# Kernel tuning notes

Hardware: AMD Instinct MI355X
Metric: run time of the kernel (lower is better)

Reference implementation:

```python
import jax, jax.numpy as jnp
import numpy as np

N_AGT, N_CTX, E, D, NC = 100000, 10000, 1000000, 128, 2


def _gn(x, w, b, eps=1e-5):
    # GroupNorm(num_groups=1) on (N, C): normalize over channels, affine.
    m = jnp.mean(x, axis=-1, keepdims=True)
    v = jnp.mean((x - m) ** 2, axis=-1, keepdims=True)
    return (x - m) * jax.lax.rsqrt(v + eps) * w + b


def setup_inputs() -> dict:
    key = jax.random.key(0)
    ks = jax.random.split(key, 16)
    s = 0.05  # weight scale
    return {
        "agts": jax.random.normal(ks[0], (N_AGT, D), jnp.float32),
        "ctx": jax.random.normal(ks[1], (N_CTX, D), jnp.float32),
        "agt_ctrs": jax.random.normal(ks[2], (N_AGT, NC), jnp.float32),
        "ctx_ctrs": jax.random.normal(ks[3], (N_CTX, NC), jnp.float32),
        "hi": jax.random.randint(ks[4], (E,), 0, N_AGT, jnp.int32),
        "wi": jax.random.randint(ks[5], (E,), 0, N_CTX, jnp.int32),
        "dist_w1": jax.random.normal(ks[6], (D, NC), jnp.float32) * s,
        "dist_b1": jnp.zeros((D,), jnp.float32),
        "dist_w2": jax.random.normal(ks[7], (D, D), jnp.float32) * s,
        "dist_gw": jnp.ones((D,), jnp.float32),
        "dist_gb": jnp.zeros((D,), jnp.float32),
        "q_w": jax.random.normal(ks[8], (D, D), jnp.float32) * s,
        "q_gw": jnp.ones((D,), jnp.float32),
        "q_gb": jnp.zeros((D,), jnp.float32),
        "ctx_w1": jax.random.normal(ks[9], (D, 3 * D), jnp.float32) * s,
        "ctx_gw": jnp.ones((D,), jnp.float32),
        "ctx_gb": jnp.zeros((D,), jnp.float32),
        "ctx_w2": jax.random.normal(ks[10], (D, D), jnp.float32) * s,
        "agt_w": jax.random.normal(ks[11], (D, D), jnp.float32) * s,
        "norm_gw": jnp.ones((D,), jnp.float32),
        "norm_gb": jnp.zeros((D,), jnp.float32),
        "lin_w": jax.random.normal(ks[12], (D, D), jnp.float32) * s,
        "lin_gw": jnp.ones((D,), jnp.float32),
        "lin_gb": jnp.zeros((D,), jnp.float32),
    }


def reference(agts, ctx, agt_ctrs, ctx_ctrs, hi, wi,
              dist_w1, dist_b1, dist_w2, dist_gw, dist_gb,
              q_w, q_gw, q_gb,
              ctx_w1, ctx_gw, ctx_gb, ctx_w2,
              agt_w, norm_gw, norm_gb,
              lin_w, lin_gw, lin_gb):
    res = agts
    # per-edge relative displacement: [E, 2]
    d = agt_ctrs[hi] - ctx_ctrs[wi]
    # dist MLP: Linear(2,128)+ReLU, Linear(128,128,nobias)+GN+ReLU
    d = jax.nn.relu(d @ dist_w1.T + dist_b1)
    d = jax.nn.relu(_gn(d @ dist_w2.T, dist_gw, dist_gb))
    # query: Linear(128,128,nobias)+GN+ReLU on gathered agents
    q = jax.nn.relu(_gn(agts[hi] @ q_w.T, q_gw, q_gb))
    # concat-MLP over edges: [E, 384] -> [E, 128]
    c = jnp.concatenate([d, q, ctx[wi]], axis=1)
    c = jax.nn.relu(_gn(c @ ctx_w1.T, ctx_gw, ctx_gb))
    c = c @ ctx_w2.T
    # agent transform + index_add scatter of edge messages
    a = agts @ agt_w.T
    a = a.at[hi].add(c)
    a = jax.nn.relu(_gn(a, norm_gw, norm_gb))
    a = _gn(a @ lin_w.T, lin_gw, lin_gb)  # Linear block with act=False
    a = jax.nn.relu(a + res)
    return a
```

## Files before the change

kernel.cpp:

```cpp
#include <hip/hip_runtime.h>
#include <stdint.h>


#define N_AGT 100000
#define N_CTX 10000
#define NE    1000000
#define D     128

typedef __attribute__((ext_vector_type(8))) __bf16 bf16x8;
typedef __attribute__((ext_vector_type(4))) float f32x4;
typedef __attribute__((ext_vector_type(4))) unsigned int uint32x4;
typedef __attribute__((ext_vector_type(8))) unsigned short ushort8;

__device__ __forceinline__ float bf_lo(uint32_t u){ return __uint_as_float(u << 16); }
__device__ __forceinline__ float bf_hi(uint32_t u){ return __uint_as_float(u & 0xFFFF0000u); }
__device__ __forceinline__ uint16_t f2bf(float f){
  uint32_t u = __float_as_uint(f);
  u += 0x7FFFu + ((u >> 16) & 1u);
  return (uint16_t)(u >> 16);
}
__device__ __forceinline__ uint16_t f2bf_fast(float f){
  const __bf16 b = (__bf16)f;
  return __builtin_bit_cast(uint16_t, b);
}
__device__ __forceinline__ float bf2f(uint16_t v){ return __uint_as_float(((uint32_t)v) << 16); }

__device__ __forceinline__ f32x4 mfma16(bf16x8 a, bf16x8 b, f32x4 c){
  return __builtin_amdgcn_mfma_f32_16x16x32_bf16(a, b, c, 0, 0, 0);
}

__device__ __forceinline__ void wave_lgkm0(){
  asm volatile("s_waitcnt lgkmcnt(0)" ::: "memory");
  __builtin_amdgcn_sched_barrier(0);
}


__device__ __forceinline__ void stage_wsz(char* dst, const float* __restrict__ W,
                                          int rs, int co, int tid, int nthr){
  for (int idx = tid; idx < 128*16; idx += nthr){
    const int row = idx >> 4, ch = idx & 15;
    const float4 f0 = *(const float4*)(W + (size_t)row*rs + co + ch*8);
    const float4 f1 = *(const float4*)(W + (size_t)row*rs + co + ch*8 + 4);
    ushort8 u;
    u[0]=f2bf(f0.x); u[1]=f2bf(f0.y); u[2]=f2bf(f0.z); u[3]=f2bf(f0.w);
    u[4]=f2bf(f1.x); u[5]=f2bf(f1.y); u[6]=f2bf(f1.z); u[7]=f2bf(f1.w);
    *(uint32x4*)(dst + row*256 + ((ch*16) ^ ((row&7)<<4))) = __builtin_bit_cast(uint32x4, u);
  }
}

__device__ __forceinline__ bf16x8 ldfrag(const char* base, int row, int cb){
  return __builtin_bit_cast(bf16x8,
      *(const uint32x4*)(base + row*256 + (cb ^ ((row&7)<<4))));
}

#define SCAN_B  256
#define SCAN_CH ((N_AGT + SCAN_B - 1) / SCAN_B)

__global__ __launch_bounds__(256) void k_hist(const int* __restrict__ hi,
                                              int* __restrict__ cnt){
  for (int i = blockIdx.x*256 + threadIdx.x; i < NE; i += gridDim.x*256)
    atomicAdd(&cnt[hi[i]], 1);
}

__global__ __launch_bounds__(256) void k_scan1(const int* __restrict__ cnt,
                                               int* __restrict__ bsum){
  __shared__ int red[4];
  const int b = blockIdx.x, t = threadIdx.x;
  const int lo = b*SCAN_CH, hiX = min(lo + SCAN_CH, N_AGT);
  int s = 0;
  for (int i = lo + t; i < hiX; i += 256) s += cnt[i];
  #pragma unroll
  for (int m = 1; m < 64; m <<= 1) s += __shfl_xor(s, m);
  if ((t & 63) == 0) red[t >> 6] = s;
  __syncthreads();
  if (t == 0) bsum[b] = red[0] + red[1] + red[2] + red[3];
}

__global__ __launch_bounds__(SCAN_B) void k_scan2(int* __restrict__ bsum){
  __shared__ int part[SCAN_B];
  const int t = threadIdx.x;
  const int v = bsum[t];
  part[t] = v;
  __syncthreads();
  for (int ofs = 1; ofs < SCAN_B; ofs <<= 1){
    const int add = (t >= ofs) ? part[t - ofs] : 0;
    __syncthreads();
    part[t] += add;
    __syncthreads();
  }
  bsum[t] = part[t] - v;
}

__global__ __launch_bounds__(256) void k_scan3(int* __restrict__ cnt,
                                               const int* __restrict__ bsum){
  __shared__ int tpart[256];
  const int b = blockIdx.x, t = threadIdx.x;
  const int lo = b*SCAN_CH, hiX = min(lo + SCAN_CH, N_AGT);
  const int per = (SCAN_CH + 255) / 256;
  const int s0 = lo + t*per, s1 = min(s0 + per, hiX);
  int s = 0;
  for (int i = s0; i < s1; i++) s += cnt[i];
  tpart[t] = s;
  __syncthreads();
  for (int ofs = 1; ofs < 256; ofs <<= 1){
    const int add = (t >= ofs) ? tpart[t - ofs] : 0;
    __syncthreads();
    tpart[t] += add;
    __syncthreads();
  }
  int run = bsum[b] + tpart[t] - s;
  for (int i = s0; i < s1; i++){
    const int c = cnt[i];
    cnt[i] = run;
    run += c;
  }
}

__global__ __launch_bounds__(256) void k_scatter(const int* __restrict__ hi,
                                                 const int* __restrict__ wi,
                                                 int* __restrict__ cur,
                                                 uint64_t* __restrict__ hw){
  for (int i = blockIdx.x*256 + threadIdx.x; i < NE; i += gridDim.x*256){
    const int h = hi[i];
    const int pos = atomicAdd(&cur[h], 1);
    hw[pos] = ((uint64_t)(uint32_t)wi[i] << 32) | (uint32_t)h;
  }
}

#define NWIT (NE/16)

__device__ __forceinline__ void mm16(const char* T, const char* W,
                                     int llo, int lhi, f32x4 acc[8]){
  bf16x8 a[4];
  #pragma unroll
  for (int kt = 0; kt < 4; kt++) a[kt] = ldfrag(T, llo, kt*64 + lhi*16);
  #pragma unroll
  for (int nt = 0; nt < 8; nt++){
    acc[nt] = (f32x4)0.f;
    #pragma unroll
    for (int kt = 0; kt < 4; kt++){
      const bf16x8 b = ldfrag(W, nt*16 + llo, kt*64 + lhi*16);
      acc[nt] = mfma16(a[kt], b, acc[nt]);
    }
  }
}

__device__ __forceinline__ void gn_reg(f32x4 acc[8], const float gw[8],
                                       const float gb[8]){
  float s[4] = {0,0,0,0}, ss[4] = {0,0,0,0};
  #pragma unroll
  for (int nt = 0; nt < 8; nt++)
    #pragma unroll
    for (int r = 0; r < 4; r++){
      const float v = acc[nt][r];
      s[r] += v; ss[r] += v*v;
    }
  #pragma unroll
  for (int m = 1; m < 16; m <<= 1)
    #pragma unroll
    for (int r = 0; r < 4; r++){
      s[r] += __shfl_xor(s[r], m);
      ss[r] += __shfl_xor(ss[r], m);
    }
  float mean[4], rstd[4];
  #pragma unroll
  for (int r = 0; r < 4; r++){
    mean[r] = s[r]*(1.f/128.f);
    const float var = ss[r]*(1.f/128.f) - mean[r]*mean[r];
    rstd[r] = rsqrtf(var + 1e-5f);
  }
  #pragma unroll
  for (int nt = 0; nt < 8; nt++)
    #pragma unroll
    for (int r = 0; r < 4; r++)
      acc[nt][r] = fmaxf((acc[nt][r]-mean[r])*rstd[r]*gw[nt] + gb[nt], 0.f);
}

__device__ __forceinline__ void scat16(char* T, const f32x4 acc[8],
                                       int llo, int lhi){
  #pragma unroll
  for (int nt = 0; nt < 8; nt++)
    #pragma unroll
    for (int r = 0; r < 4; r++){
      const int row = lhi*4 + r;
      *(uint16_t*)(T + row*256 + ((2*(nt*16 + llo)) ^ ((row&7)<<4))) =
          f2bf_fast(acc[nt][r]);
    }
}

__global__ __launch_bounds__(512, 2) void k_edge_mfma(
    const float* __restrict__ agt_ctrs, const float* __restrict__ ctx_ctrs,
    const uint32_t* __restrict__ hw32,
    const float* __restrict__ dist_w1, const float* __restrict__ dist_b1,
    const float* __restrict__ dist_gw, const float* __restrict__ dist_gb,
    const float* __restrict__ ctx_gw, const float* __restrict__ ctx_gb,
    const float* __restrict__ dist_w2, const float* __restrict__ ctx_w1,
    const float* __restrict__ ctx_w2,
    const uint16_t* __restrict__ QW, const uint16_t* __restrict__ CtxP,
    float* __restrict__ A0){
  extern __shared__ __align__(16) char smem[];
  const int tid  = threadIdx.x;
  const int wave = tid >> 6, lane = tid & 63;
  const int lhi  = lane >> 4, llo = lane & 15;

  stage_wsz(smem,         dist_w2, 128, 0, tid, 512);
  stage_wsz(smem + 32768, ctx_w1,  384, 0, tid, 512);
  stage_wsz(smem + 65536, ctx_w2,  128, 0, tid, 512);

  char* T = smem + 98304 + wave*4096;

  const int c0 = llo*8;
  float w1x[8], w1y[8], b1v[8];
  #pragma unroll
  for (int j = 0; j < 8; j++){
    w1x[j] = dist_w1[(c0+j)*2 + 0];
    w1y[j] = dist_w1[(c0+j)*2 + 1];
    b1v[j] = dist_b1[c0+j];
  }
  float dgwr[8], dgbr[8], cgwr[8], cgbr[8];
  #pragma unroll
  for (int nt = 0; nt < 8; nt++){
    dgwr[nt] = dist_gw[nt*16 + llo]; dgbr[nt] = dist_gb[nt*16 + llo];
    cgwr[nt] = ctx_gw[nt*16 + llo];  cgbr[nt] = ctx_gb[nt*16 + llo];
  }
  __syncthreads();

  const int wid = blockIdx.x*8 + wave;
  const int nw  = gridDim.x*8;

  for (int i = wid; i < NWIT; i += nw){
    const int base = i*16;
    const uint32x4 q0 = *(const uint32x4*)&hw32[2*(base + lhi*4)];
    const uint32x4 q1 = *(const uint32x4*)&hw32[2*(base + lhi*4) + 4];
    const int hh[4] = {(int)q0[0], (int)q0[2], (int)q1[0], (int)q1[2]};
    const int ww[4] = {(int)q0[1], (int)q0[3], (int)q1[1], (int)q1[3]};
    const uint2 p2 = *(const uint2*)&hw32[2*(base + llo)];
    const int h2 = (int)p2.x, w2 = (int)p2.y;
    uint32x4 qql[4], qcl[4];
    #pragma unroll
    for (int k = 0; k < 4; k++){
      qql[k] = *(const uint32x4*)&QW  [(size_t)h2*D + lhi*32 + k*8];
      qcl[k] = *(const uint32x4*)&CtxP[(size_t)w2*D + lhi*32 + k*8];
    }
    #pragma unroll
    for (int j = 0; j < 4; j++){
      const float2 ac = *(const float2*)&agt_ctrs[(size_t)hh[j]*2];
      const float2 cc = *(const float2*)&ctx_ctrs[(size_t)ww[j]*2];
      const float dx = ac.x - cc.x, dy = ac.y - cc.y;
      ushort8 u;
      #pragma unroll
      for (int c = 0; c < 8; c++)
        u[c] = f2bf_fast(fmaxf(fmaf(dx, w1x[c], fmaf(dy, w1y[c], b1v[c])), 0.f));
      const int row = lhi*4 + j;
      *(uint32x4*)(T + row*256 + ((llo*16) ^ ((row&7)<<4))) =
          __builtin_bit_cast(uint32x4, u);
    }
    wave_lgkm0();
    f32x4 acc[8];
    mm16(T, smem, llo, lhi, acc);
    gn_reg(acc, dgwr, dgbr);
    wave_lgkm0();
    scat16(T, acc, llo, lhi);
    wave_lgkm0();
    mm16(T, smem + 32768, llo, lhi, acc);
    ushort8 qs[4];
    #pragma unroll
    for (int k = 0; k < 4; k++){
      const ushort8 a = __builtin_bit_cast(ushort8, qql[k]);
      const ushort8 b = __builtin_bit_cast(ushort8, qcl[k]);
      ushort8 v;
      #pragma unroll
      for (int j = 0; j < 8; j++) v[j] = f2bf_fast(bf2f(a[j]) + bf2f(b[j]));
      qs[k] = v;
    }
    wave_lgkm0();
    #pragma unroll
    for (int k = 0; k < 4; k++)
      *(uint32x4*)(T + llo*256 + (((lhi*64) + k*16) ^ ((llo&7)<<4))) =
          __builtin_bit_cast(uint32x4, qs[k]);
    wave_lgkm0();
    #pragma unroll
    for (int nt = 0; nt < 8; nt++)
      #pragma unroll
      for (int r = 0; r < 4; r++){
        const int row = lhi*4 + r;
        const uint16_t q = *(const uint16_t*)(T + row*256 +
            ((2*(nt*16 + llo)) ^ ((row&7)<<4)));
        acc[nt][r] += bf2f(q);
      }
    gn_reg(acc, cgwr, cgbr);
    wave_lgkm0();
    scat16(T, acc, llo, lhi);
    wave_lgkm0();
    mm16(T, smem + 65536, llo, lhi, acc);
    wave_lgkm0();
    scat16(T, acc, llo, lhi);
    wave_lgkm0();
    {
      const int cA = lane, cB = lane + 64;
      float runA = 0.f, runB = 0.f;
      int hprev = __shfl(h2, 0);
      #pragma unroll
      for (int k = 0; k < 16; k++){
        const int hk = __shfl(h2, k);
        if (hk != hprev){
          atomicAdd(&A0[(size_t)hprev*D + cA], runA);
          atomicAdd(&A0[(size_t)hprev*D + cB], runB);
          runA = 0.f; runB = 0.f; hprev = hk;
        }
        runA += bf2f(*(const uint16_t*)(T + k*256 + ((2*cA) ^ ((k&7)<<4))));
        runB += bf2f(*(const uint16_t*)(T + k*256 + ((2*cB) ^ ((k&7)<<4))));
      }
      atomicAdd(&A0[(size_t)hprev*D + cA], runA);
      atomicAdd(&A0[(size_t)hprev*D + cB], runB);
    }
  }
}

__device__ __forceinline__ void mm_stage(const char* xb, const char* wm, int wv,
                                         int llo, int lhi, f32x4 acc[3][2]){
  #pragma unroll
  for (int kt = 0; kt < 4; kt++){
    const int cb = kt*64 + lhi*16;
    const bf16x8 b0 = ldfrag(wm, wv*32 + llo,      cb);
    const bf16x8 b1 = ldfrag(wm, wv*32 + 16 + llo, cb);
    #pragma unroll
    for (int mt = 0; mt < 3; mt++){
      const bf16x8 a = ldfrag(xb, mt*16 + llo, cb);
      acc[mt][0] = mfma16(a, b0, acc[mt][0]);
      acc[mt][1] = mfma16(a, b1, acc[mt][1]);
    }
  }
}

__device__ __forceinline__ void scat_acc(char* xb, const f32x4 acc[3][2],
                                         int wv, int llo, int lhi){
  #pragma unroll
  for (int mt = 0; mt < 3; mt++)
    #pragma unroll
    for (int ntl = 0; ntl < 2; ntl++)
      #pragma unroll
      for (int r = 0; r < 4; r++){
        const int m = mt*16 + lhi*4 + r;
        const int n = wv*32 + ntl*16 + llo;
        *(uint16_t*)(xb + m*256 + ((n*2) ^ ((m&7)<<4))) = f2bf(acc[mt][ntl][r]);
      }
}

__device__ __forceinline__ void gn_rowpass(char* xb, const int rr[3], int llo,
                                           const float gw[8], const float gb[8]){
  #pragma unroll
  for (int i = 0; i < 3; i++){
    const int row = rr[i];
    char* p = xb + row*256 + ((llo*16) ^ ((row&7)<<4));
    ushort8 u = __builtin_bit_cast(ushort8, *(const uint32x4*)p);
    float f[8]; float s = 0.f, ss = 0.f;
    #pragma unroll
    for (int j = 0; j < 8; j++){ f[j] = bf2f(u[j]); s += f[j]; ss += f[j]*f[j]; }
    #pragma unroll
    for (int m = 1; m < 16; m <<= 1){ s += __shfl_xor(s, m); ss += __shfl_xor(ss, m); }
    const float mean = s*(1.f/128.f);
    const float var  = ss*(1.f/128.f) - mean*mean;
    const float rstd = rsqrtf(var + 1e-5f);
    #pragma unroll
    for (int j = 0; j < 8; j++){
      const float g = fmaxf((f[j]-mean)*rstd*gw[j] + gb[j], 0.f);
      u[j] = f2bf(g);
    }
    *(uint32x4*)p = __builtin_bit_cast(uint32x4, u);
  }
}

#define NITER_A ((N_AGT + 95) / 96)

__global__ __launch_bounds__(512, 2) void k_agent_pre_mfma(
    const float* __restrict__ agts, const float* __restrict__ q_w,
    const float* __restrict__ ctx_w1, const float* __restrict__ agt_w,
    const float* __restrict__ q_gw, const float* __restrict__ q_gb,
    uint16_t* __restrict__ QW, float* __restrict__ A0){
  extern __shared__ __align__(16) char smem[];
  const int tid  = threadIdx.x;
  const int wave = tid >> 6, lane = tid & 63;
  const int grp  = wave >> 2, wv = wave & 3;
  const int lhi  = lane >> 4, llo = lane & 15;

  stage_wsz(smem,         q_w,    128, 0,   tid, 512);
  stage_wsz(smem + 32768, agt_w,  128, 0,   tid, 512);
  stage_wsz(smem + 65536, ctx_w1, 384, 128, tid, 512);

  char* xb = smem + 98304 + grp*12288;
  const int c0 = llo*8;
  float qgw[8], qgb[8];
  #pragma unroll
  for (int j = 0; j < 8; j++){ qgw[j] = q_gw[c0+j]; qgb[j] = q_gb[c0+j]; }
  __syncthreads();

  const int tg = tid & 255;
  int rr[3];
  #pragma unroll
  for (int i = 0; i < 3; i++) rr[i] = wv*12 + i*4 + lhi;

  for (int it = blockIdx.x; it < NITER_A; it += gridDim.x){
    const int rbase = it*96 + grp*48;
    for (int idx = tg; idx < 48*32; idx += 256){
      const int row = idx >> 5, c4 = idx & 31;
      int gr = rbase + row; if (gr >= N_AGT) gr = N_AGT - 1;
      const float4 f = *(const float4*)(agts + (size_t)gr*D + c4*4);
      const uint32_t lo = ((uint32_t)f2bf(f.y) << 16) | (uint32_t)f2bf(f.x);
      const uint32_t hi2 = ((uint32_t)f2bf(f.w) << 16) | (uint32_t)f2bf(f.z);
      *(uint2*)(xb + row*256 + ((c4*8) ^ ((row&7)<<4))) = make_uint2(lo, hi2);
    }
    __syncthreads();
    f32x4 acc[3][2];
    #pragma unroll
    for (int mt = 0; mt < 3; mt++){ acc[mt][0] = (f32x4)0.f; acc[mt][1] = (f32x4)0.f; }
    mm_stage(xb, smem + 32768, wv, llo, lhi, acc);
    #pragma unroll
    for (int mt = 0; mt < 3; mt++)
      #pragma unroll
      for (int ntl = 0; ntl < 2; ntl++)
        #pragma unroll
        for (int r = 0; r < 4; r++){
          const int m = mt*16 + lhi*4 + r;
          if (rbase + m < N_AGT){
            const int n = wv*32 + ntl*16 + llo;
            A0[(size_t)(rbase + m)*D + n] = acc[mt][ntl][r];
          }
        }
    #pragma unroll
    for (int mt = 0; mt < 3; mt++){ acc[mt][0] = (f32x4)0.f; acc[mt][1] = (f32x4)0.f; }
    mm_stage(xb, smem, wv, llo, lhi, acc);
    __syncthreads();
    scat_acc(xb, acc, wv, llo, lhi);
    __syncthreads();
    gn_rowpass(xb, rr, llo, qgw, qgb);
    __syncthreads();
    #pragma unroll
    for (int mt = 0; mt < 3; mt++){ acc[mt][0] = (f32x4)0.f; acc[mt][1] = (f32x4)0.f; }
    mm_stage(xb, smem + 65536, wv, llo, lhi, acc);
    __syncthreads();
    scat_acc(xb, acc, wv, llo, lhi);
    __syncthreads();
    #pragma unroll
    for (int i = 0; i < 3; i++){
      const int row = rr[i], gr = rbase + row;
      if (gr < N_AGT){
        const uint32x4 u = *(const uint32x4*)(xb + row*256 + ((llo*16) ^ ((row&7)<<4)));
        *(uint32x4*)(QW + (size_t)gr*D + c0) = u;
      }
    }
    __syncthreads();
  }
}

__global__ __launch_bounds__(512, 4) void k_post_mfma(
    float* __restrict__ A0, const float* __restrict__ agts,
    const float* __restrict__ lin_w,
    const float* __restrict__ norm_gw, const float* __restrict__ norm_gb,
    const float* __restrict__ lin_gw, const float* __restrict__ lin_gb){
  extern __shared__ __align__(16) char smem[];
  const int tid  = threadIdx.x;
  const int wave = tid >> 6, lane = tid & 63;
  const int grp  = wave >> 2, wv = wave & 3;
  const int lhi  = lane >> 4, llo = lane & 15;

  stage_wsz(smem, lin_w, 128, 0, tid, 512);
  char* xb = smem + 32768 + grp*12288;
  const int c0 = llo*8;
  float ngw[8], ngb[8], lgw[8], lgb[8];
  #pragma unroll
  for (int j = 0; j < 8; j++){
    ngw[j] = norm_gw[c0+j]; ngb[j] = norm_gb[c0+j];
    lgw[j] = lin_gw[c0+j];  lgb[j] = lin_gb[c0+j];
  }
  __syncthreads();

  int rr[3];
  #pragma unroll
  for (int i = 0; i < 3; i++) rr[i] = wv*12 + i*4 + lhi;

  for (int it = blockIdx.x; it < NITER_A; it += gridDim.x){
    const int rbase = it*96 + grp*48;
    #pragma unroll
    for (int i = 0; i < 3; i++){
      const int row = rr[i];
      int gr = rbase + row; if (gr >= N_AGT) gr = N_AGT - 1;
      const float4 a0 = *(const float4*)(A0 + (size_t)gr*D + c0);
      const float4 a1 = *(const float4*)(A0 + (size_t)gr*D + c0 + 4);
      float f[8] = {a0.x,a0.y,a0.z,a0.w,a1.x,a1.y,a1.z,a1.w};
      float s = 0.f, ss = 0.f;
      #pragma unroll
      for (int j = 0; j < 8; j++){ s += f[j]; ss += f[j]*f[j]; }
      #pragma unroll
      for (int m = 1; m < 16; m <<= 1){ s += __shfl_xor(s, m); ss += __shfl_xor(ss, m); }
      const float mean = s*(1.f/128.f);
      const float var  = ss*(1.f/128.f) - mean*mean;
      const float rstd = rsqrtf(var + 1e-5f);
      ushort8 u;
      #pragma unroll
      for (int j = 0; j < 8; j++)
        u[j] = f2bf(fmaxf((f[j]-mean)*rstd*ngw[j] + ngb[j], 0.f));
      *(uint32x4*)(xb + row*256 + ((llo*16) ^ ((row&7)<<4))) =
          __builtin_bit_cast(uint32x4, u);
    }
    __syncthreads();
    f32x4 acc[3][2];
    #pragma unroll
    for (int mt = 0; mt < 3; mt++){ acc[mt][0] = (f32x4)0.f; acc[mt][1] = (f32x4)0.f; }
    mm_stage(xb, smem, wv, llo, lhi, acc);
    __syncthreads();
    scat_acc(xb, acc, wv, llo, lhi);
    __syncthreads();
    #pragma unroll
    for (int i = 0; i < 3; i++){
      const int row = rr[i];
      const char* p = xb + row*256 + ((llo*16) ^ ((row&7)<<4));
      const ushort8 u = __builtin_bit_cast(ushort8, *(const uint32x4*)p);
      float f[8]; float s = 0.f, ss = 0.f;
      #pragma unroll
      for (int j = 0; j < 8; j++){ f[j] = bf2f(u[j]); s += f[j]; ss += f[j]*f[j]; }
      #pragma unroll
      for (int m = 1; m < 16; m <<= 1){ s += __shfl_xor(s, m); ss += __shfl_xor(ss, m); }
      const float mean = s*(1.f/128.f);
      const float var  = ss*(1.f/128.f) - mean*mean;
      const float rstd = rsqrtf(var + 1e-5f);
      const int gr = rbase + row;
      if (gr < N_AGT){
        const float4 r0 = *(const float4*)(agts + (size_t)gr*D + c0);
        const float4 r1 = *(const float4*)(agts + (size_t)gr*D + c0 + 4);
        const float res[8] = {r0.x,r0.y,r0.z,r0.w,r1.x,r1.y,r1.z,r1.w};
        float o[8];
        float4 o0, o1;
        #pragma unroll
        for (int j = 0; j < 8; j++)
          o[j] = fmaxf((f[j]-mean)*rstd*lgw[j] + lgb[j] + res[j], 0.f);
        o0.x=o[0]; o0.y=o[1]; o0.z=o[2]; o0.w=o[3];
        o1.x=o[4]; o1.y=o[5]; o1.z=o[6]; o1.w=o[7];
        *(float4*)(A0 + (size_t)gr*D + c0)     = o0;
        *(float4*)(A0 + (size_t)gr*D + c0 + 4) = o1;
      }
    }
    __syncthreads();
  }
}

__device__ __forceinline__ void stage_w4(uint32_t* wp, const float* __restrict__ W,
                                         int rs, int co, int tid, int nthr){
  for (int idx = tid; idx < 32*128; idx += nthr){
    int p2 = idx & 31, o = idx >> 5;
    const float4 f = *(const float4*)(W + (size_t)o*rs + co + p2*4);
    uint32_t lo = ((uint32_t)f2bf(f.y) << 16) | (uint32_t)f2bf(f.x);
    uint32_t hi = ((uint32_t)f2bf(f.w) << 16) | (uint32_t)f2bf(f.z);
    *(uint2*)&wp[(p2*128 + o)*2] = make_uint2(lo, hi);
  }
}

__device__ __forceinline__ float dot128(const uint32_t* wp, const float* xb, int o){
  float acc = 0.f;
  #pragma unroll 8
  for (int p2 = 0; p2 < 32; p2++){
    const uint2 w = *(const uint2*)&wp[(p2*128 + o)*2];
    const float4 x = *(const float4*)&xb[p2*4];
    acc += x.x*bf_lo(w.x) + x.y*bf_hi(w.x) + x.z*bf_lo(w.y) + x.w*bf_hi(w.y);
  }
  return acc;
}

__global__ __launch_bounds__(128) void k_ctx(const float* __restrict__ ctx,
                                             const float* __restrict__ ctx_w1,
                                             uint16_t* __restrict__ CtxP){
  __shared__ __align__(16) uint32_t wc[32*128*2];
  __shared__ __align__(16) float xbuf[128];
  const int tid = threadIdx.x;
  stage_w4(wc, ctx_w1, 384, 256, tid, 128);
  __syncthreads();
  for (int row = blockIdx.x; row < N_CTX; row += gridDim.x){
    __syncthreads();
    xbuf[tid] = ctx[(size_t)row*D + tid];
    __syncthreads();
    const float acc = dot128(wc, xbuf, tid);
    CtxP[(size_t)row*D + tid] = f2bf(acc);
  }
}

extern "C" void kernel_launch(void* const* d_in, const int* in_sizes, int n_in,
                              void* d_out, int out_size, void* d_ws, size_t ws_size,
                              hipStream_t stream){
  const float* agts     = (const float*)d_in[0];
  const float* ctx      = (const float*)d_in[1];
  const float* agt_ctrs = (const float*)d_in[2];
  const float* ctx_ctrs = (const float*)d_in[3];
  const int*   hi       = (const int*)d_in[4];
  const int*   wi       = (const int*)d_in[5];
  const float* dist_w1  = (const float*)d_in[6];
  const float* dist_b1  = (const float*)d_in[7];
  const float* dist_w2  = (const float*)d_in[8];
  const float* dist_gw  = (const float*)d_in[9];
  const float* dist_gb  = (const float*)d_in[10];
  const float* q_w      = (const float*)d_in[11];
  const float* q_gw     = (const float*)d_in[12];
  const float* q_gb     = (const float*)d_in[13];
  const float* ctx_w1   = (const float*)d_in[14];
  const float* ctx_gw   = (const float*)d_in[15];
  const float* ctx_gb   = (const float*)d_in[16];
  const float* ctx_w2   = (const float*)d_in[17];
  const float* agt_w    = (const float*)d_in[18];
  const float* norm_gw  = (const float*)d_in[19];
  const float* norm_gb  = (const float*)d_in[20];
  const float* lin_w    = (const float*)d_in[21];
  const float* lin_gw   = (const float*)d_in[22];
  const float* lin_gb   = (const float*)d_in[23];

  uint16_t* QW   = (uint16_t*)d_ws;
  uint16_t* CtxP = QW + (size_t)N_AGT * D;
  int*      cnt  = (int*)((char*)d_ws + 28160000);
  int*      bsum = (int*)((char*)d_ws + 28560000);
  uint64_t* hw   = (uint64_t*)((char*)d_ws + 28561024);
  float*    A0   = (float*)d_out;

  const int EDGE_LDS = 131072;
  const int APRE_LDS = 122880;
  const int POST_LDS = 57344;
  hipFuncSetAttribute((const void*)k_edge_mfma,
                      hipFuncAttributeMaxDynamicSharedMemorySize, EDGE_LDS);
  hipFuncSetAttribute((const void*)k_agent_pre_mfma,
                      hipFuncAttributeMaxDynamicSharedMemorySize, APRE_LDS);
  hipFuncSetAttribute((const void*)k_post_mfma,
                      hipFuncAttributeMaxDynamicSharedMemorySize, POST_LDS);

  hipMemsetAsync(cnt, 0, (size_t)N_AGT*4, stream);
  k_hist<<<2048, 256, 0, stream>>>(hi, cnt);
  k_scan1<<<SCAN_B, 256, 0, stream>>>(cnt, bsum);
  k_scan2<<<1, SCAN_B, 0, stream>>>(bsum);
  k_scan3<<<SCAN_B, 256, 0, stream>>>(cnt, bsum);
  k_scatter<<<2048, 256, 0, stream>>>(hi, wi, cnt, hw);

  k_ctx<<<1024, 128, 0, stream>>>(ctx, ctx_w1, CtxP);
  k_agent_pre_mfma<<<256, 512, APRE_LDS, stream>>>(agts, q_w, ctx_w1, agt_w,
      q_gw, q_gb, QW, A0);
  k_edge_mfma<<<256, 512, EDGE_LDS, stream>>>(agt_ctrs, ctx_ctrs,
      (const uint32_t*)hw,
      dist_w1, dist_b1, dist_gw, dist_gb, ctx_gw, ctx_gb,
      dist_w2, ctx_w1, ctx_w2, QW, CtxP, A0);
  k_post_mfma<<<512, 512, POST_LDS, stream>>>(A0, agts, lin_w,
      norm_gw, norm_gb, lin_gw, lin_gb);
}
```

Measured before the change: 581.4 us.

## Software-pipeline edge gathers by prefetching next iteration's indices and rows

The edge loop now loads the next tile's edge indices, gathered QW/CtxP rows and centre coordinates during the current tile's matmul and GN stages, then rotates them into place at the end of the iteration. This is meant to hide global gather latency behind MFMA and LDS work in the persistent wave loop. It raises register pressure, with extra uint32x4 arrays and float2s held live, which could lower occupancy or cause spills.

```diff
diff --git a/kernel.cpp b/kernel.cpp
--- a/kernel.cpp
+++ b/kernel.cpp
@@ -228,15 +228,19 @@
   const int wid = blockIdx.x*8 + wave;
   const int nw  = gridDim.x*8;
 
-  for (int i = wid; i < NWIT; i += nw){
-    const int base = i*16;
+  int h2, w2;
+  float2 acs[4], ccs[4];
+  int hh[4], ww[4];
+  uint32x4 qql[4], qcl[4];
+
+  if (wid < NWIT){
+    const int base = wid*16;
     const uint32x4 q0 = *(const uint32x4*)&hw32[2*(base + lhi*4)];
     const uint32x4 q1 = *(const uint32x4*)&hw32[2*(base + lhi*4) + 4];
-    const int hh[4] = {(int)q0[0], (int)q0[2], (int)q1[0], (int)q1[2]};
-    const int ww[4] = {(int)q0[1], (int)q0[3], (int)q1[1], (int)q1[3]};
+    hh[0]=(int)q0[0]; hh[1]=(int)q0[2]; hh[2]=(int)q1[0]; hh[3]=(int)q1[2];
+    ww[0]=(int)q0[1]; ww[1]=(int)q0[3]; ww[2]=(int)q1[1]; ww[3]=(int)q1[3];
     const uint2 p2 = *(const uint2*)&hw32[2*(base + llo)];
-    const int h2 = (int)p2.x, w2 = (int)p2.y;
-    uint32x4 qql[4], qcl[4];
+    h2 = (int)p2.x; w2 = (int)p2.y;
     #pragma unroll
     for (int k = 0; k < 4; k++){
       qql[k] = *(const uint32x4*)&QW  [(size_t)h2*D + lhi*32 + k*8];
@@ -244,9 +248,16 @@
     }
     #pragma unroll
     for (int j = 0; j < 4; j++){
-      const float2 ac = *(const float2*)&agt_ctrs[(size_t)hh[j]*2];
-      const float2 cc = *(const float2*)&ctx_ctrs[(size_t)ww[j]*2];
-      const float dx = ac.x - cc.x, dy = ac.y - cc.y;
+      acs[j] = *(const float2*)&agt_ctrs[(size_t)hh[j]*2];
+      ccs[j] = *(const float2*)&ctx_ctrs[(size_t)ww[j]*2];
+    }
+  }
+
+  for (int i = wid; i < NWIT; i += nw){
+    const bool hasn = (i + nw) < NWIT;
+    #pragma unroll
+    for (int j = 0; j < 4; j++){
+      const float dx = acs[j].x - ccs[j].x, dy = acs[j].y - ccs[j].y;
       ushort8 u;
       #pragma unroll
       for (int c = 0; c < 8; c++)
@@ -255,12 +266,37 @@
       *(uint32x4*)(T + row*256 + ((llo*16) ^ ((row&7)<<4))) =
           __builtin_bit_cast(uint32x4, u);
     }
+    uint32x4 q0n, q1n; uint2 p2n;
+    if (hasn){
+      const int nb = (i + nw)*16;
+      q0n = *(const uint32x4*)&hw32[2*(nb + lhi*4)];
+      q1n = *(const uint32x4*)&hw32[2*(nb + lhi*4) + 4];
+      p2n = *(const uint2*)&hw32[2*(nb + llo)];
+    }
     wave_lgkm0();
     f32x4 acc[8];
     mm16(T, smem, llo, lhi, acc);
     gn_reg(acc, dgwr, dgbr);
     wave_lgkm0();
     scat16(T, acc, llo, lhi);
+    int h2n = 0, w2n = 0, hhn[4], wwn[4];
+    uint32x4 qqln[4], qcln[4];
+    float2 acsn[4], ccsn[4];
+    if (hasn){
+      hhn[0]=(int)q0n[0]; hhn[1]=(int)q0n[2]; hhn[2]=(int)q1n[0]; hhn[3]=(int)q1n[2];
+      wwn[0]=(int)q0n[1]; wwn[1]=(int)q0n[3]; wwn[2]=(int)q1n[1]; wwn[3]=(int)q1n[3];
+      h2n = (int)p2n.x; w2n = (int)p2n.y;
+      #pragma unroll
+      for (int k = 0; k < 4; k++){
+        qqln[k] = *(const uint32x4*)&QW  [(size_t)h2n*D + lhi*32 + k*8];
+        qcln[k] = *(const uint32x4*)&CtxP[(size_t)w2n*D + lhi*32 + k*8];
+      }
+      #pragma unroll
+      for (int j = 0; j < 4; j++){
+        acsn[j] = *(const float2*)&agt_ctrs[(size_t)hhn[j]*2];
+        ccsn[j] = *(const float2*)&ctx_ctrs[(size_t)wwn[j]*2];
+      }
+    }
     wave_lgkm0();
     mm16(T, smem + 32768, llo, lhi, acc);
     ushort8 qs[4];
@@ -313,6 +349,16 @@
       }
       atomicAdd(&A0[(size_t)hprev*D + cA], runA);
       atomicAdd(&A0[(size_t)hprev*D + cB], runB);
+    }
+    if (hasn){
+      h2 = h2n; w2 = w2n;
+      #pragma unroll
+      for (int j = 0; j < 4; j++){
+        hh[j] = hhn[j]; ww[j] = wwn[j];
+        acs[j] = acsn[j]; ccs[j] = ccsn[j];
+      }
+      #pragma unroll
+      for (int k = 0; k < 4; k++){ qql[k] = qqln[k]; qcl[k] = qcln[k]; }
     }
   }
 }
```

Measured after the change: 933.0 us. +60.5%, slower.

## Read ctx weights from global bf16 copies to halve edge kernel LDS

Applied to the files above, without the earlier changes.

Adds a small prep kernel that converts ctx_w1 and ctx_w2 to swizzled bf16 buffers in workspace. The edge kernel now reads those fragments directly from global memory instead of staging them in LDS. This cuts LDS use from 128KB to 64KB and doubles the grid, aiming for more resident blocks per CU. In exchange, the MFMA weight loads move from LDS to the cache hierarchy with higher latency.

```diff
diff --git a/kernel.cpp b/kernel.cpp
--- a/kernel.cpp
+++ b/kernel.cpp
@@ -51,6 +51,25 @@
 __device__ __forceinline__ bf16x8 ldfrag(const char* base, int row, int cb){
   return __builtin_bit_cast(bf16x8,
       *(const uint32x4*)(base + row*256 + (cb ^ ((row&7)<<4))));
+}
+
+__global__ __launch_bounds__(256) void k_wprep(const float* __restrict__ ctx_w1,
+                                               const float* __restrict__ ctx_w2,
+                                               char* __restrict__ w1dg,
+                                               char* __restrict__ wc2g){
+  const int t = blockIdx.x*256 + threadIdx.x;
+  if (t >= 2*2048) return;
+  const int m = t >> 11, idx = t & 2047;
+  const float* W = m ? ctx_w2 : ctx_w1;
+  const int rs = m ? 128 : 384;
+  char* dst = m ? wc2g : w1dg;
+  const int row = idx >> 4, ch = idx & 15;
+  const float4 f0 = *(const float4*)(W + (size_t)row*rs + ch*8);
+  const float4 f1 = *(const float4*)(W + (size_t)row*rs + ch*8 + 4);
+  ushort8 u;
+  u[0]=f2bf(f0.x); u[1]=f2bf(f0.y); u[2]=f2bf(f0.z); u[3]=f2bf(f0.w);
+  u[4]=f2bf(f1.x); u[5]=f2bf(f1.y); u[6]=f2bf(f1.z); u[7]=f2bf(f1.w);
+  *(uint32x4*)(dst + row*256 + ((ch*16) ^ ((row&7)<<4))) = __builtin_bit_cast(uint32x4, u);
 }
 
 #define SCAN_B  256
@@ -194,8 +213,8 @@
     const float* __restrict__ dist_w1, const float* __restrict__ dist_b1,
     const float* __restrict__ dist_gw, const float* __restrict__ dist_gb,
     const float* __restrict__ ctx_gw, const float* __restrict__ ctx_gb,
-    const float* __restrict__ dist_w2, const float* __restrict__ ctx_w1,
-    const float* __restrict__ ctx_w2,
+    const float* __restrict__ dist_w2,
+    const char* __restrict__ w1dg, const char* __restrict__ wc2g,
     const uint16_t* __restrict__ QW, const uint16_t* __restrict__ CtxP,
     float* __restrict__ A0){
   extern __shared__ __align__(16) char smem[];
@@ -203,11 +222,9 @@
   const int wave = tid >> 6, lane = tid & 63;
   const int lhi  = lane >> 4, llo = lane & 15;
 
-  stage_wsz(smem,         dist_w2, 128, 0, tid, 512);
-  stage_wsz(smem + 32768, ctx_w1,  384, 0, tid, 512);
-  stage_wsz(smem + 65536, ctx_w2,  128, 0, tid, 512);
-
-  char* T = smem + 98304 + wave*4096;
+  stage_wsz(smem, dist_w2, 128, 0, tid, 512);
+
+  char* T = smem + 32768 + wave*4096;
 
   const int c0 = llo*8;
   float w1x[8], w1y[8], b1v[8];
@@ -262,7 +279,7 @@
     wave_lgkm0();
     scat16(T, acc, llo, lhi);
     wave_lgkm0();
-    mm16(T, smem + 32768, llo, lhi, acc);
+    mm16(T, w1dg, llo, lhi, acc);
     ushort8 qs[4];
     #pragma unroll
     for (int k = 0; k < 4; k++){
@@ -292,7 +309,7 @@
     wave_lgkm0();
     scat16(T, acc, llo, lhi);
     wave_lgkm0();
-    mm16(T, smem + 65536, llo, lhi, acc);
+    mm16(T, wc2g, llo, lhi, acc);
     wave_lgkm0();
     scat16(T, acc, llo, lhi);
     wave_lgkm0();
@@ -616,9 +633,11 @@
   int*      cnt  = (int*)((char*)d_ws + 28160000);
   int*      bsum = (int*)((char*)d_ws + 28560000);
   uint64_t* hw   = (uint64_t*)((char*)d_ws + 28561024);
+  char*     w1dg = (char*)d_ws + 36561024;
+  char*     wc2g = (char*)d_ws + 36593792;
   float*    A0   = (float*)d_out;
 
-  const int EDGE_LDS = 131072;
+  const int EDGE_LDS = 65536;
   const int APRE_LDS = 122880;
   const int POST_LDS = 57344;
   hipFuncSetAttribute((const void*)k_edge_mfma,
@@ -630,6 +649,7 @@
 
   hipMemsetAsync(cnt, 0, (size_t)N_AGT*4, stream);
   k_hist<<<2048, 256, 0, stream>>>(hi, cnt);
+  k_wprep<<<16, 256, 0, stream>>>(ctx_w1, ctx_w2, w1dg, wc2g);
   k_scan1<<<SCAN_B, 256, 0, stream>>>(cnt, bsum);
   k_scan2<<<1, SCAN_B, 0, stream>>>(bsum);
   k_scan3<<<SCAN_B, 256, 0, stream>>>(cnt, bsum);
@@ -638,10 +658,10 @@
   k_ctx<<<1024, 128, 0, stream>>>(ctx, ctx_w1, CtxP);
   k_agent_pre_mfma<<<256, 512, APRE_LDS, stream>>>(agts, q_w, ctx_w1, agt_w,
       q_gw, q_gb, QW, A0);
-  k_edge_mfma<<<256, 512, EDGE_LDS, stream>>>(agt_ctrs, ctx_ctrs,
+  k_edge_mfma<<<512, 512, EDGE_LDS, stream>>>(agt_ctrs, ctx_ctrs,
       (const uint32_t*)hw,
       dist_w1, dist_b1, dist_gw, dist_gb, ctx_gw, ctx_gb,
-      dist_w2, ctx_w1, ctx_w2, QW, CtxP, A0);
+      dist_w2, w1dg, wc2g, QW, CtxP, A0);
   k_post_mfma<<<512, 512, POST_LDS, stream>>>(A0, agts, lin_w,
       norm_gw, norm_gb, lin_gw, lin_gb);
 }
```

Result: slower. 1.330 ms (+128.8%).
